# Optimization experiments

Measured on AMD Instinct MI355X. Metric: run time of the kernel, lower is better.

The kernel has to match this reference:

```python
import jax, jax.numpy as jnp
from jax import lax
import numpy as np

S = 0.7071067811865476  # 1/sqrt(2), pywt haar filter coefficient


def dwt2(x):
    """Single-level 2D Haar DWT over last two axes, pywt convention.
    Returns (cA, cH, cV, cD) with cH='da' (row detail), cV='ad' (col detail)."""
    lo = (x[..., 0::2, :] + x[..., 1::2, :]) * S  # low-pass along rows (axis -2)
    hi = (x[..., 0::2, :] - x[..., 1::2, :]) * S  # high-pass along rows
    cA = (lo[..., 0::2] + lo[..., 1::2]) * S      # 'aa'
    cV = (lo[..., 0::2] - lo[..., 1::2]) * S      # 'ad'
    cH = (hi[..., 0::2] + hi[..., 1::2]) * S      # 'da'
    cD = (hi[..., 0::2] - hi[..., 1::2]) * S      # 'dd'
    return cA, cH, cV, cD


def _interleave(e, o, axis):
    s = jnp.stack([e, o], axis=axis)
    shp = list(e.shape)
    shp[axis] = shp[axis] * 2 if axis >= 0 else shp[axis] * 2
    # move to explicit positive handling
    out_shape = list(e.shape)
    out_shape[axis % e.ndim] *= 2
    return s.reshape(out_shape)


def idwt2(cA, cH, cV, cD):
    """Inverse of dwt2 (Haar, perfect reconstruction)."""
    # undo column transform
    lo_e = (cA + cV) * S
    lo_o = (cA - cV) * S
    lo = jnp.stack([lo_e, lo_o], axis=-1).reshape(cA.shape[:-1] + (cA.shape[-1] * 2,))
    hi_e = (cH + cD) * S
    hi_o = (cH - cD) * S
    hi = jnp.stack([hi_e, hi_o], axis=-1).reshape(cH.shape[:-1] + (cH.shape[-1] * 2,))
    # undo row transform
    r_e = (lo + hi) * S  # even rows
    r_o = (lo - hi) * S  # odd rows
    B = lo.shape[:-2]
    H2, W = lo.shape[-2], lo.shape[-1]
    x = jnp.stack([r_e, r_o], axis=-2).reshape(B + (2 * H2, W))
    return x


def batchnorm_relu(x, gamma, beta, eps=1e-5):
    """BatchNorm2d in training mode (biased batch stats over N,H,W) + ReLU."""
    mean = jnp.mean(x, axis=(0, 2, 3), keepdims=True)
    var = jnp.var(x, axis=(0, 2, 3), keepdims=True)
    xn = (x - mean) * lax.rsqrt(var + eps)
    return jax.nn.relu(xn * gamma[None, :, None, None] + beta[None, :, None, None])


def setup_inputs() -> dict:
    key = jax.random.key(0)
    ks = jax.random.split(key, 4)
    return {
        "x": jax.random.normal(ks[0], (16, 256, 64, 64), dtype=jnp.float32),
        "conv_w": jax.random.normal(ks[1], (256, 256), dtype=jnp.float32) * 0.05,
        "bn_gamma": jnp.ones((256,), jnp.float32),
        "bn_beta": jnp.zeros((256,), jnp.float32),
        "convW_w": jax.random.normal(ks[2], (256, 512, 3, 3), dtype=jnp.float32) * 0.02,
        "convW_b": jnp.zeros((256,), jnp.float32),
        "bnW_gamma": jnp.ones((256,), jnp.float32),
        "bnW_beta": jnp.zeros((256,), jnp.float32),
    }


def reference(x, conv_w, bn_gamma, bn_beta, convW_w, convW_b, bnW_gamma, bnW_beta):
    # Branch 0: single-level DWT, per-subband 1x1 conv + BN + ReLU, then IDWT.
    cA, cH, cV, cD = dwt2(x)
    proc = lambda c: batchnorm_relu(jnp.einsum('bchw,oc->bohw', c, conv_w), bn_gamma, bn_beta)
    rimg0 = idwt2(proc(cA), proc(cH), proc(cV), proc(cD))  # [B,256,H,W]

    # Branch 1: level-3 wavedec2 then full reconstruction (identity up to fp error).
    a1, h1, v1, d1 = dwt2(x)
    a2, h2, v2, d2 = dwt2(a1)
    a3, h3, v3, d3 = dwt2(a2)
    r3 = idwt2(a3, h3, v3, d3)
    r2 = idwt2(r3, h2, v2, d2)
    rimg1 = idwt2(r2, h1, v1, d1)  # [B,256,H,W]

    rimg = jnp.concatenate([rimg0, rimg1], axis=1)  # [B,512,H,W]
    y = lax.conv_general_dilated(
        rimg, convW_w, window_strides=(1, 1), padding='SAME',
        dimension_numbers=('NCHW', 'OIHW', 'NCHW'))
    y = y + convW_b[None, :, None, None]
    return batchnorm_relu(y, bnW_gamma, bnW_beta)
```

## Files before the change

kernel.cpp:

```cpp
#include <hip/hip_runtime.h>
#include <hip/hip_bf16.h>

#define SQ2 0.70710678118654752440f

typedef __attribute__((ext_vector_type(4))) float f32x4;
typedef __attribute__((ext_vector_type(16))) float f32x16;
typedef __attribute__((ext_vector_type(8))) short s16x8;


__device__ __forceinline__ unsigned short f2bf(float f){
  unsigned u = __builtin_bit_cast(unsigned, f);
  u += 0x7FFFu + ((u >> 16) & 1u);
  return (unsigned short)(u >> 16);
}

__device__ __forceinline__ void gload16(const void* g, const void* l){
  __builtin_amdgcn_global_load_lds((const __attribute__((address_space(1))) void*)g,
                                   (__attribute__((address_space(3))) void*)l, 16, 0, 0);
}

__global__ void k_cvt_cw(const float* __restrict__ w, unsigned short* __restrict__ o){
  int g = blockIdx.x * blockDim.x + threadIdx.x;
  if (g < 256*256) o[g] = f2bf(w[g]);
}

__global__ void k_cvt_wb(const float* __restrict__ w, unsigned short* __restrict__ o){
  const int N = 256*512*9;
  for (int g = blockIdx.x*blockDim.x + threadIdx.x; g < N; g += gridDim.x*blockDim.x){
    int tap = g % 9;
    int t2  = g / 9;
    int cin = t2 & 511;
    int oc  = t2 >> 9;
    o[(tap*256 + oc)*512 + cin] = f2bf(w[g]);
  }
}

__global__ __launch_bounds__(256) void k_x_nhwc(const float* __restrict__ x,
                                                unsigned short* __restrict__ Cb){
  __shared__ float tile[32][65];
  int bh = blockIdx.x;
  int b = bh >> 6, h = bh & 63;
  int t = threadIdx.x;
  for (int cc = 0; cc < 256; cc += 32){
    int w = t & 63, c4 = t >> 6;
#pragma unroll
    for (int r = 0; r < 8; ++r){
      int c = c4*8 + r;
      tile[c][w] = x[((b*256 + cc + c)*64 + h)*64 + w];
    }
    __syncthreads();
    int c = t & 31, w4 = t >> 5;
#pragma unroll
    for (int r = 0; r < 8; ++r){
      int w2 = w4*8 + r;
      Cb[((b*64 + h)*64 + w2)*512 + 256 + cc + c] = f2bf(tile[c][w2]);
    }
    __syncthreads();
  }
}

__global__ __launch_bounds__(256) void k_gemm1_dwt(const unsigned short* __restrict__ Cb,
                                                   const unsigned short* __restrict__ cw,
                                                   float* __restrict__ sub){
  int d = blockIdx.x;
  int xcd = d & 7, idx = d >> 3;
  int b = xcd*2 + (idx >> 7);
  int rest = idx & 127;
  int rp = rest >> 2, ot = rest & 3;
  int tid = threadIdx.x, wave = tid >> 6, l = tid & 63;
  int l16 = l & 15, lg = l >> 4;
  int obase = ot * 64;
  f32x4 acc[2][4];
#pragma unroll
  for (int i = 0; i < 2; ++i)
#pragma unroll
    for (int j = 0; j < 4; ++j) acc[i][j] = (f32x4)0.0f;

  for (int cc = 0; cc < 256; cc += 32){
    s16x8 a[2], bf[4];
#pragma unroll
    for (int mt = 0; mt < 2; ++mt){
      int p  = wave*32 + mt*16 + l16;
      int w  = p >> 1, rr = p & 1;
      int hin = rp*2 + rr;
      a[mt] = *(const s16x8*)(Cb + ((b*64 + hin)*64 + w)*512 + 256 + cc + lg*8);
    }
#pragma unroll
    for (int nt = 0; nt < 4; ++nt){
      int o = obase + nt*16 + l16;
      bf[nt] = *(const s16x8*)(cw + o*256 + cc + lg*8);
    }
#pragma unroll
    for (int mt = 0; mt < 2; ++mt)
#pragma unroll
      for (int nt = 0; nt < 4; ++nt)
        acc[mt][nt] = __builtin_amdgcn_mfma_f32_16x16x32_bf16(a[mt], bf[nt], acc[mt][nt], 0, 0, 0);
  }

#pragma unroll
  for (int mt = 0; mt < 2; ++mt){
    int j = wave*8 + mt*4 + lg;
#pragma unroll
    for (int nt = 0; nt < 4; ++nt){
      int o = obase + nt*16 + l16;
      f32x4 v = acc[mt][nt];
      float lo0 = (v.x + v.y)*SQ2, hi0 = (v.x - v.y)*SQ2;
      float lo1 = (v.z + v.w)*SQ2, hi1 = (v.z - v.w)*SQ2;
      float cA = (lo0 + lo1)*SQ2, cV = (lo0 - lo1)*SQ2;
      float cH = (hi0 + hi1)*SQ2, cD = (hi0 - hi1)*SQ2;
      int base = ((b*32 + rp)*32 + j)*256 + o;
      sub[base]              = cA;
      sub[base +   4194304]  = cH;
      sub[base + 2*4194304]  = cV;
      sub[base + 3*4194304]  = cD;
    }
  }
}

__global__ __launch_bounds__(256) void k_stats_sub(const float* __restrict__ sub,
                                                   float* __restrict__ statsA){
  int bx = blockIdx.x;
  int pg = bx & 7, b = (bx >> 3) & 15, s = bx >> 7;
  int t = threadIdx.x;
  const float* base = sub + (size_t)(s*16 + b)*262144 + pg*128*256;
  float sum = 0.f, sq = 0.f;
  for (int pos = 0; pos < 128; ++pos){
    float v = base[pos*256 + t];
    sum += v; sq += v*v;
  }
  atomicAdd(&statsA[(s*256 + t)*2],     sum);
  atomicAdd(&statsA[(s*256 + t)*2 + 1], sq);
}

__global__ void k_fin_A(const float* __restrict__ statsA, const float* __restrict__ gamma,
                        const float* __restrict__ beta, float* __restrict__ bnA){
  int t = blockIdx.x*blockDim.x + threadIdx.x;
  if (t >= 1024) return;
  int c = t & 255;
  const float n = 16384.f;
  float mean = statsA[t*2] / n;
  float var  = statsA[t*2+1] / n - mean*mean;
  float sc = gamma[c] * rsqrtf(var + 1e-5f);
  bnA[t*2]   = sc;
  bnA[t*2+1] = beta[c] - mean*sc;
}

__global__ __launch_bounds__(256) void k_bn_idwt(const float* __restrict__ sub,
                                                 const float* __restrict__ bnA,
                                                 unsigned short* __restrict__ Cb){
  int bx = blockIdx.x;
  int b = bx >> 5, i = bx & 31;
  int c = threadIdx.x;
  float scA = bnA[c*2],              shA = bnA[c*2+1];
  float scH = bnA[(256+c)*2],        shH = bnA[(256+c)*2+1];
  float scV = bnA[(512+c)*2],        shV = bnA[(512+c)*2+1];
  float scD = bnA[(768+c)*2],        shD = bnA[(768+c)*2+1];
  for (int j = 0; j < 32; ++j){
    size_t idx = ((size_t)(b*32 + i)*32 + j)*256 + c;
    float a  = fmaxf(sub[idx]              * scA + shA, 0.f);
    float hh = fmaxf(sub[idx +   4194304]  * scH + shH, 0.f);
    float v  = fmaxf(sub[idx + 2*4194304]  * scV + shV, 0.f);
    float d  = fmaxf(sub[idx + 3*4194304]  * scD + shD, 0.f);
    float lo_e = (a + v)*SQ2, lo_o = (a - v)*SQ2;
    float hi_e = (hh + d)*SQ2, hi_o = (hh - d)*SQ2;
    int h2 = 2*i, w2 = 2*j;
    Cb[((b*64 + h2  )*64 + w2  )*512 + c] = f2bf((lo_e + hi_e)*SQ2);
    Cb[((b*64 + h2  )*64 + w2+1)*512 + c] = f2bf((lo_o + hi_o)*SQ2);
    Cb[((b*64 + h2+1)*64 + w2  )*512 + c] = f2bf((lo_e - hi_e)*SQ2);
    Cb[((b*64 + h2+1)*64 + w2+1)*512 + c] = f2bf((lo_o - hi_o)*SQ2);
  }
}

__global__ __launch_bounds__(512, 2) void k_conv3(const unsigned short* __restrict__ Cb,
                                                  const unsigned short* __restrict__ Wb,
                                                  const unsigned short* __restrict__ guard,
                                                  const float* __restrict__ bias,
                                                  float* __restrict__ y){
  __shared__ char sm[50176];

  int d = blockIdx.x;
  int xcd = d & 7, idx = d >> 3;
  int b  = xcd*2 + (idx >> 4);
  int r  = idx & 15;
  int rg = r >> 1;
  int cg = r & 1;
  int h0 = rg*8, c0 = cg*32;

  int tid = threadIdx.x, wv = tid >> 6, l = tid & 63;
  int l32 = l & 31, lh = l >> 5;
  int wo = wv >> 1, wp = wv & 1;

  if (tid < 256) *(float*)(sm + 49152 + tid*4) = bias[tid];

  const unsigned short* ip[2];
  int iadv[2], ilds[2];
#pragma unroll
  for (int k = 0; k < 2; ++k){
    int j = (wv + 8*k)*64 + l;
    ilds[k] = j*16;
    const unsigned short* p = guard; int adv = 0;
    if (j < 680){
      int lgp = j / 340, pp = j % 340;
      int rr = pp / 34, c = pp % 34;
      int hin = h0 - 1 + rr, win = c0 - 1 + c;
      if ((unsigned)hin < 64u && (unsigned)win < 64u){
        p = Cb + (((b*64 + hin)*64 + win)*512 + lgp*8);
        adv = 16;
      }
    }
    ip[k] = p; iadv[k] = adv;
  }

  int jw = wv*64 + l;
  const unsigned short* wg = Wb + (jw & 255)*512 + (jw >> 8)*8;
  int wlds = jw*16;

  f32x16 acc[2][4];
#pragma unroll
  for (int mt = 0; mt < 2; ++mt)
#pragma unroll
    for (int nt = 0; nt < 4; ++nt) acc[mt][nt] = (f32x16)0.0f;

  gload16(ip[0], sm + ilds[0]);
  gload16(ip[1], sm + ilds[1]);
  gload16(wg,    sm + 32768 + wlds);
  __syncthreads();

  int scpar = 0;
  for (int sc = 0; sc < 32; ++sc){
    char* ibc = sm + scpar*16384;
    char* ibn = sm + (scpar^1)*16384;
#pragma unroll
    for (int tau = 0; tau < 9; ++tau){
      int wpar = (scpar + tau) & 1;
      char* wbc = sm + 32768 + wpar*8192;
      char* wbn = sm + 32768 + (wpar^1)*8192;

      __builtin_amdgcn_s_barrier();
      if (tau < 8) gload16(wg + (tau+1)*131072, wbn + wlds);
      else         gload16(wg + 16,             wbn + wlds);
      if (tau == 7){
        ip[0] += iadv[0]; ip[1] += iadv[1];
        gload16(ip[0], ibn + ilds[0]);
        gload16(ip[1], ibn + ilds[1]);
      }
      if (tau == 8) asm volatile("s_waitcnt vmcnt(3)" ::: "memory");
      else          asm volatile("s_waitcnt vmcnt(1)" ::: "memory");
      __builtin_amdgcn_s_barrier();

      const int kh = tau / 3, kw = tau % 3;
      s16x8 A[2], Bf[4];
#pragma unroll
      for (int mt = 0; mt < 2; ++mt)
        A[mt] = *(const s16x8*)(wbc + (lh*256 + wo*64 + mt*32 + l32)*16);
#pragma unroll
      for (int nt = 0; nt < 4; ++nt)
        Bf[nt] = *(const s16x8*)(ibc + (lh*340 + (wp*4 + nt + kh)*34 + l32 + kw)*16);
      __builtin_amdgcn_s_setprio(1);
#pragma unroll
      for (int mt = 0; mt < 2; ++mt)
#pragma unroll
        for (int nt = 0; nt < 4; ++nt)
          acc[mt][nt] = __builtin_amdgcn_mfma_f32_32x32x16_bf16(A[mt], Bf[nt], acc[mt][nt], 0, 0, 0);
      __builtin_amdgcn_s_setprio(0);
    }
    wg += 16;
    scpar ^= 1;
  }

#pragma unroll
  for (int mt = 0; mt < 2; ++mt){
#pragma unroll
    for (int nt = 0; nt < 4; ++nt){
      int pr = wp*4 + nt, pc = l32;
      f32x16 v = acc[mt][nt];
#pragma unroll
      for (int rr = 0; rr < 16; ++rr){
        int row = (rr & 3) + 8*(rr >> 2) + 4*lh;
        int o = wo*64 + mt*32 + row;
        float bo = *(const float*)(sm + 49152 + o*4);
        y[((b*256 + o)*64 + (h0 + pr))*64 + c0 + pc] = v[rr] + bo;
      }
    }
  }
}

__global__ __launch_bounds__(256) void k_stats_y(const float* __restrict__ y,
                                                 const float* __restrict__ g,
                                                 const float* __restrict__ be,
                                                 float* __restrict__ bnY){
  int o = blockIdx.x;
  int t = threadIdx.x;
  float sum = 0.f, sq = 0.f;
  for (int idx = t; idx < 16384; idx += 256){
    int bb = idx >> 10, p4 = idx & 1023;
    f32x4 v = *(const f32x4*)(y + (size_t)(bb*256 + o)*4096 + p4*4);
    sum += v.x + v.y + v.z + v.w;
    sq  += v.x*v.x + v.y*v.y + v.z*v.z + v.w*v.w;
  }
  __shared__ float s1[256], s2[256];
  s1[t] = sum; s2[t] = sq;
  __syncthreads();
  for (int off = 128; off; off >>= 1){
    if (t < off){ s1[t] += s1[t+off]; s2[t] += s2[t+off]; }
    __syncthreads();
  }
  if (t == 0){
    const float n = 65536.f;
    float mean = s1[0] / n;
    float var  = s2[0] / n - mean*mean;
    float sc = g[o] * rsqrtf(var + 1e-5f);
    bnY[o*2]   = sc;
    bnY[o*2+1] = be[o] - mean*sc;
  }
}

__global__ __launch_bounds__(256) void k_bn_out(float* __restrict__ y,
                                                const float* __restrict__ bnY){
  int gI = blockIdx.x*256 + threadIdx.x;
  int o = (gI >> 10) & 255;
  float sc = bnY[o*2], sh = bnY[o*2+1];
  f32x4 v = ((const f32x4*)y)[gI];
  v.x = fmaxf(v.x*sc + sh, 0.f);
  v.y = fmaxf(v.y*sc + sh, 0.f);
  v.z = fmaxf(v.z*sc + sh, 0.f);
  v.w = fmaxf(v.w*sc + sh, 0.f);
  ((f32x4*)y)[gI] = v;
}

extern "C" void kernel_launch(void* const* d_in, const int* in_sizes, int n_in,
                              void* d_out, int out_size, void* d_ws, size_t ws_size,
                              hipStream_t stream) {
  const float* x       = (const float*)d_in[0];
  const float* conv_w  = (const float*)d_in[1];
  const float* bn_g    = (const float*)d_in[2];
  const float* bn_b    = (const float*)d_in[3];
  const float* convW_w = (const float*)d_in[4];
  const float* convW_b = (const float*)d_in[5];
  const float* bnW_g   = (const float*)d_in[6];
  const float* bnW_b   = (const float*)d_in[7];
  float* out = (float*)d_out;

  unsigned char* base = (unsigned char*)d_ws;
  unsigned short* Cb   = (unsigned short*)base;
  unsigned short* cw_b = (unsigned short*)(base + (64u<<20));
  unsigned short* Wb   = (unsigned short*)(base + (64u<<20) + (1u<<20));
  unsigned short* guard= (unsigned short*)(base + (67u<<20) + (512u<<10));
  float* statsA        = (float*)(base + (68u<<20));
  float* bnA           = statsA + 2048;
  float* bnY           = bnA + 2048;

  float* sub = out;

  hipLaunchKernelGGL(k_cvt_cw, dim3(256), dim3(256), 0, stream, conv_w, cw_b);
  hipLaunchKernelGGL(k_cvt_wb, dim3(1152), dim3(256), 0, stream, convW_w, Wb);
  hipLaunchKernelGGL(k_x_nhwc, dim3(1024), dim3(256), 0, stream, x, Cb);
  hipMemsetAsync(statsA, 0, 4*256*2*sizeof(float), stream);
  hipMemsetAsync(guard, 0, 256, stream);
  hipLaunchKernelGGL(k_gemm1_dwt, dim3(2048), dim3(256), 0, stream, Cb, cw_b, sub);
  hipLaunchKernelGGL(k_stats_sub, dim3(512), dim3(256), 0, stream, sub, statsA);
  hipLaunchKernelGGL(k_fin_A, dim3(4), dim3(256), 0, stream, statsA, bn_g, bn_b, bnA);
  hipLaunchKernelGGL(k_bn_idwt, dim3(512), dim3(256), 0, stream, sub, bnA, Cb);
  hipLaunchKernelGGL(k_conv3, dim3(256), dim3(512), 0, stream, Cb, Wb, guard, convW_b, out);
  hipLaunchKernelGGL(k_stats_y, dim3(256), dim3(256), 0, stream, out, bnW_g, bnW_b, bnY);
  hipLaunchKernelGGL(k_bn_out, dim3(16384), dim3(256), 0, stream, out, bnY);
}
```

Measured before the change: 423.7 us.

## Retile 3x3 conv into smaller blocks and fuse output BN stats via atomics

New measurement: 642.0 us. 1.52x slower.

```diff
diff --git a/kernel.cpp b/kernel.cpp
--- a/kernel.cpp
+++ b/kernel.cpp
@@ -171,148 +171,117 @@
   }
 }
 
-__global__ __launch_bounds__(512, 2) void k_conv3(const unsigned short* __restrict__ Cb,
+__global__ __launch_bounds__(512, 4) void k_conv3(const unsigned short* __restrict__ Cb,
                                                   const unsigned short* __restrict__ Wb,
                                                   const unsigned short* __restrict__ guard,
                                                   const float* __restrict__ bias,
-                                                  float* __restrict__ y){
-  __shared__ char sm[50176];
+                                                  float* __restrict__ y,
+                                                  float* __restrict__ statsY){
+  __shared__ char sm[36864];
 
   int d = blockIdx.x;
   int xcd = d & 7, idx = d >> 3;
-  int b  = xcd*2 + (idx >> 4);
-  int r  = idx & 15;
-  int rg = r >> 1;
-  int cg = r & 1;
-  int h0 = rg*8, c0 = cg*32;
+  int b   = xcd*2 + (idx >> 6);
+  int rem = idx & 63;
+  int rg = rem >> 2, og = rem & 3;
+  int h0 = rg*4, obase = og*64;
 
   int tid = threadIdx.x, wv = tid >> 6, l = tid & 63;
   int l32 = l & 31, lh = l >> 5;
-  int wo = wv >> 1, wp = wv & 1;
-
-  if (tid < 256) *(float*)(sm + 49152 + tid*4) = bias[tid];
-
-  const unsigned short* ip[2];
-  int iadv[2], ilds[2];
+  int wo = wv & 1, wp = wv >> 1;
+
+  const unsigned short* ip[2]; int iadv[2];
 #pragma unroll
   for (int k = 0; k < 2; ++k){
-    int j = (wv + 8*k)*64 + l;
-    ilds[k] = j*16;
+    int j = tid + 512*k;
     const unsigned short* p = guard; int adv = 0;
-    if (j < 680){
-      int lgp = j / 340, pp = j % 340;
-      int rr = pp / 34, c = pp % 34;
-      int hin = h0 - 1 + rr, win = c0 - 1 + c;
+    if (j < 792){
+      int pl = j/396, q = j%396, rr = q/66, c = q%66;
+      int hin = h0 - 1 + rr, win = c - 1;
       if ((unsigned)hin < 64u && (unsigned)win < 64u){
-        p = Cb + (((b*64 + hin)*64 + win)*512 + lgp*8);
+        p = Cb + (((b*64 + hin)*64 + win)*512 + pl*8);
         adv = 16;
       }
     }
     ip[k] = p; iadv[k] = adv;
   }
 
-  int jw = wv*64 + l;
-  const unsigned short* wg = Wb + (jw & 255)*512 + (jw >> 8)*8;
-  int wlds = jw*16;
-
-  f32x16 acc[2][4];
-#pragma unroll
-  for (int mt = 0; mt < 2; ++mt)
-#pragma unroll
-    for (int nt = 0; nt < 4; ++nt) acc[mt][nt] = (f32x16)0.0f;
-
-  gload16(ip[0], sm + ilds[0]);
-  gload16(ip[1], sm + ilds[1]);
-  gload16(wg,    sm + 32768 + wlds);
-  __syncthreads();
-
-  int scpar = 0;
+  int ws  = wv*64 + l;
+  int wpl = ws >> 6, wob = ws & 63;
+  const unsigned short* wg = Wb + ((obase + wob)*512 + wpl*8);
+
+  f32x16 acc0 = (f32x16)0.0f, acc1 = (f32x16)0.0f;
+
+  gload16(ip[0], sm + tid*16);
+  gload16(ip[1], sm + 8192 + tid*16);
+  if (wv < 2) gload16(wg, sm + 32768 + ws*16);
+
+  int pp = 0;
   for (int sc = 0; sc < 32; ++sc){
-    char* ibc = sm + scpar*16384;
-    char* ibn = sm + (scpar^1)*16384;
+    char* ibc = sm + (sc & 1)*16384;
+    char* ibn = sm + ((sc & 1) ^ 1)*16384;
 #pragma unroll
     for (int tau = 0; tau < 9; ++tau){
-      int wpar = (scpar + tau) & 1;
-      char* wbc = sm + 32768 + wpar*8192;
-      char* wbn = sm + 32768 + (wpar^1)*8192;
-
+      asm volatile("s_waitcnt vmcnt(0)" ::: "memory");
       __builtin_amdgcn_s_barrier();
-      if (tau < 8) gload16(wg + (tau+1)*131072, wbn + wlds);
-      else         gload16(wg + 16,             wbn + wlds);
-      if (tau == 7){
-        ip[0] += iadv[0]; ip[1] += iadv[1];
-        gload16(ip[0], ibn + ilds[0]);
-        gload16(ip[1], ibn + ilds[1]);
+      char* wbc = sm + 32768 + pp*2048;
+      char* wbn = sm + 32768 + (pp ^ 1)*2048;
+      int p = sc*9 + tau;
+      if (p < 287){
+        int ntap = (tau < 8) ? tau + 1 : 0;
+        int nsc  = (tau < 8) ? sc : sc + 1;
+        if (wv < 2) gload16(wg + ntap*131072 + nsc*16, wbn + ws*16);
+        if (tau == 8){
+          ip[0] += iadv[0]; ip[1] += iadv[1];
+          gload16(ip[0], ibn + tid*16);
+          gload16(ip[1], ibn + 8192 + tid*16);
+        }
       }
-      if (tau == 8) asm volatile("s_waitcnt vmcnt(3)" ::: "memory");
-      else          asm volatile("s_waitcnt vmcnt(1)" ::: "memory");
-      __builtin_amdgcn_s_barrier();
-
       const int kh = tau / 3, kw = tau % 3;
-      s16x8 A[2], Bf[4];
-#pragma unroll
-      for (int mt = 0; mt < 2; ++mt)
-        A[mt] = *(const s16x8*)(wbc + (lh*256 + wo*64 + mt*32 + l32)*16);
-#pragma unroll
-      for (int nt = 0; nt < 4; ++nt)
-        Bf[nt] = *(const s16x8*)(ibc + (lh*340 + (wp*4 + nt + kh)*34 + l32 + kw)*16);
+      s16x8 A  = *(const s16x8*)(wbc + ((lh*64 + wo*32 + l32) << 4));
+      s16x8 B0 = *(const s16x8*)(ibc + ((lh*396 + (wp + kh)*66 + l32 + kw) << 4));
+      s16x8 B1 = *(const s16x8*)(ibc + ((lh*396 + (wp + kh)*66 + 32 + l32 + kw) << 4));
       __builtin_amdgcn_s_setprio(1);
-#pragma unroll
-      for (int mt = 0; mt < 2; ++mt)
-#pragma unroll
-        for (int nt = 0; nt < 4; ++nt)
-          acc[mt][nt] = __builtin_amdgcn_mfma_f32_32x32x16_bf16(A[mt], Bf[nt], acc[mt][nt], 0, 0, 0);
+      acc0 = __builtin_amdgcn_mfma_f32_32x32x16_bf16(A, B0, acc0, 0, 0, 0);
+      acc1 = __builtin_amdgcn_mfma_f32_32x32x16_bf16(A, B1, acc1, 0, 0, 0);
       __builtin_amdgcn_s_setprio(0);
-    }
-    wg += 16;
-    scpar ^= 1;
-  }
-
-#pragma unroll
-  for (int mt = 0; mt < 2; ++mt){
-#pragma unroll
-    for (int nt = 0; nt < 4; ++nt){
-      int pr = wp*4 + nt, pc = l32;
-      f32x16 v = acc[mt][nt];
-#pragma unroll
-      for (int rr = 0; rr < 16; ++rr){
-        int row = (rr & 3) + 8*(rr >> 2) + 4*lh;
-        int o = wo*64 + mt*32 + row;
-        float bo = *(const float*)(sm + 49152 + o*4);
-        y[((b*256 + o)*64 + (h0 + pr))*64 + c0 + pc] = v[rr] + bo;
-      }
-    }
-  }
-}
-
-__global__ __launch_bounds__(256) void k_stats_y(const float* __restrict__ y,
-                                                 const float* __restrict__ g,
-                                                 const float* __restrict__ be,
-                                                 float* __restrict__ bnY){
-  int o = blockIdx.x;
-  int t = threadIdx.x;
-  float sum = 0.f, sq = 0.f;
-  for (int idx = t; idx < 16384; idx += 256){
-    int bb = idx >> 10, p4 = idx & 1023;
-    f32x4 v = *(const f32x4*)(y + (size_t)(bb*256 + o)*4096 + p4*4);
-    sum += v.x + v.y + v.z + v.w;
-    sq  += v.x*v.x + v.y*v.y + v.z*v.z + v.w*v.w;
-  }
-  __shared__ float s1[256], s2[256];
-  s1[t] = sum; s2[t] = sq;
-  __syncthreads();
-  for (int off = 128; off; off >>= 1){
-    if (t < off){ s1[t] += s1[t+off]; s2[t] += s2[t+off]; }
-    __syncthreads();
-  }
-  if (t == 0){
-    const float n = 65536.f;
-    float mean = s1[0] / n;
-    float var  = s2[0] / n - mean*mean;
-    float sc = g[o] * rsqrtf(var + 1e-5f);
-    bnY[o*2]   = sc;
-    bnY[o*2+1] = be[o] - mean*sc;
-  }
+      pp ^= 1;
+    }
+  }
+
+  int h = h0 + wp;
+#pragma unroll
+  for (int rr = 0; rr < 16; ++rr){
+    int o = obase + wo*32 + (rr & 3) + 8*(rr >> 2) + 4*lh;
+    float bo = bias[o];
+    float v0 = acc0[rr] + bo;
+    float v1 = acc1[rr] + bo;
+    float* yp = y + ((size_t)(b*256 + o)*64 + h)*64;
+    yp[l32]      = v0;
+    yp[32 + l32] = v1;
+    float s = v0 + v1, q = v0*v0 + v1*v1;
+#pragma unroll
+    for (int m = 1; m < 32; m <<= 1){
+      s += __shfl_xor(s, m, 64);
+      q += __shfl_xor(q, m, 64);
+    }
+    if (l32 == 0){
+      atomicAdd(&statsY[o*2],     s);
+      atomicAdd(&statsY[o*2 + 1], q);
+    }
+  }
+}
+
+__global__ void k_fin_Y(const float* __restrict__ statsY, const float* __restrict__ g,
+                        const float* __restrict__ be, float* __restrict__ bnY){
+  int o = blockIdx.x*blockDim.x + threadIdx.x;
+  if (o >= 256) return;
+  const float n = 65536.f;
+  float mean = statsY[o*2] / n;
+  float var  = statsY[o*2+1] / n - mean*mean;
+  float sc = g[o] * rsqrtf(var + 1e-5f);
+  bnY[o*2]   = sc;
+  bnY[o*2+1] = be[o] - mean*sc;
 }
 
 __global__ __launch_bounds__(256) void k_bn_out(float* __restrict__ y,
@@ -347,7 +316,8 @@
   unsigned short* Wb   = (unsigned short*)(base + (64u<<20) + (1u<<20));
   unsigned short* guard= (unsigned short*)(base + (67u<<20) + (512u<<10));
   float* statsA        = (float*)(base + (68u<<20));
-  float* bnA           = statsA + 2048;
+  float* statsY        = statsA + 2048;
+  float* bnA           = statsA + 2560;
   float* bnY           = bnA + 2048;
 
   float* sub = out;
@@ -355,13 +325,13 @@
   hipLaunchKernelGGL(k_cvt_cw, dim3(256), dim3(256), 0, stream, conv_w, cw_b);
   hipLaunchKernelGGL(k_cvt_wb, dim3(1152), dim3(256), 0, stream, convW_w, Wb);
   hipLaunchKernelGGL(k_x_nhwc, dim3(1024), dim3(256), 0, stream, x, Cb);
-  hipMemsetAsync(statsA, 0, 4*256*2*sizeof(float), stream);
+  hipMemsetAsync(statsA, 0, 2560*sizeof(float), stream);
   hipMemsetAsync(guard, 0, 256, stream);
   hipLaunchKernelGGL(k_gemm1_dwt, dim3(2048), dim3(256), 0, stream, Cb, cw_b, sub);
   hipLaunchKernelGGL(k_stats_sub, dim3(512), dim3(256), 0, stream, sub, statsA);
   hipLaunchKernelGGL(k_fin_A, dim3(4), dim3(256), 0, stream, statsA, bn_g, bn_b, bnA);
   hipLaunchKernelGGL(k_bn_idwt, dim3(512), dim3(256), 0, stream, sub, bnA, Cb);
-  hipLaunchKernelGGL(k_conv3, dim3(256), dim3(512), 0, stream, Cb, Wb, guard, convW_b, out);
-  hipLaunchKernelGGL(k_stats_y, dim3(256), dim3(256), 0, stream, out, bnW_g, bnW_b, bnY);
+  hipLaunchKernelGGL(k_conv3, dim3(1024), dim3(512), 0, stream, Cb, Wb, guard, convW_b, out, statsY);
+  hipLaunchKernelGGL(k_fin_Y, dim3(1), dim3(256), 0, stream, statsY, bnW_g, bnW_b, bnY);
   hipLaunchKernelGGL(k_bn_out, dim3(16384), dim3(256), 0, stream, out, bnY);
 }
```
